# Optimization experiments

Hardware: AMD Instinct MI355X
Metric: run time of the kernel (lower is better)

The kernel has to match this reference:

```python
import jax, jax.numpy as jnp
import numpy as np

N, D, H, C, E = 16384, 768, 768, 2, 20

def setup_inputs() -> dict:
    key = jax.random.key(0)
    k1, k2, k3, k4, k5, k6 = jax.random.split(key, 6)
    return {
        "embeddings": jax.random.normal(k1, (N, D), dtype=jnp.float32),
        "component_idx": jax.random.randint(k2, (N,), 0, E, dtype=jnp.int64),
        "W1": jax.random.normal(k3, (E, D, H), dtype=jnp.float32) * (1.0 / np.sqrt(D)),
        "b1": jnp.zeros((E, H), dtype=jnp.float32),
        "W2": jax.random.normal(k4, (E, H, C), dtype=jnp.float32) * (1.0 / np.sqrt(H)),
        "b2": jnp.zeros((E, C), dtype=jnp.float32),
    }

def reference(embeddings, component_idx, W1, b1, W2, b2):
    # Each token n goes through expert component_idx[n]:
    #   y = relu(x @ W1[e] + b1[e]) @ W2[e] + b2[e]
    # The torch module's mask/cat/argsort reassembly is mathematically a
    # per-token select of its own expert's output at the original position.
    # Dense-expert formulation (standard jax MoE fallback), then gather.
    h = jax.nn.relu(jnp.einsum('nd,edh->enh', embeddings, W1) + b1[:, None, :])  # [E,N,H]
    y = jnp.einsum('enh,ehc->enc', h, W2) + b2[:, None, :]                        # [E,N,C]
    n_idx = jnp.arange(embeddings.shape[0])
    return y[component_idx, n_idx]  # [N,C]
```

## Files before the change

### kernel.cpp

```cpp
#include <hip/hip_runtime.h>

#define N_D 768
#define N_H 768
#define N_C 2
#define N_E 20
#define MT 128
#define NT 128
#define BK 32
#define KT (N_D / BK)
#define MAX_TILES 160
#define NCOL (N_H / NT)
#define ROWB (N_D * 2)
#define W1BLKS (N_E * (N_D / 64) * (N_H / 64))
#define XBBLKS 256

typedef __attribute__((ext_vector_type(8))) short short8;
typedef __attribute__((ext_vector_type(4))) float f32x4;

__device__ __forceinline__ unsigned short f2bf(float f) {
  unsigned u = __builtin_bit_cast(unsigned, f);
  u += 0x7FFFu + ((u >> 16) & 1u);
  return (unsigned short)(u >> 16);
}

#define GLD_LDS16(gp, lp)                                                        \
  __builtin_amdgcn_global_load_lds(                                              \
      (const __attribute__((address_space(1))) void*)(gp),                       \
      (__attribute__((address_space(3))) void*)(lp), 16, 0, 0)


__global__ __launch_bounds__(256) void k_prep(
    const int* __restrict__ cidx, int* __restrict__ counts,
    int* __restrict__ offsets, int* __restrict__ tiles,
    int* __restrict__ numTiles, int* __restrict__ sorted,
    const float* __restrict__ emb, unsigned short* __restrict__ Xb,
    const float* __restrict__ W1, unsigned short* __restrict__ W1t,
    float* __restrict__ out, int n) {
  const int tid = threadIdx.x;

  if (blockIdx.x == 0) {
    __shared__ int lc[4][N_E];
    __shared__ int tot[N_E];
    __shared__ int scur[N_E];
    const int w = tid >> 6;
    for (int k = tid; k < 4 * N_E; k += 256) ((int*)lc)[k] = 0;
    __syncthreads();
    const int4* c4 = (const int4*)cidx;
    const int nv = n >> 2;
    for (int i = tid; i < nv; i += 256) {
      int4 v = c4[i];
      int e0 = v.x < 0 ? 0 : (v.x >= N_E ? N_E - 1 : v.x);
      int e1 = v.y < 0 ? 0 : (v.y >= N_E ? N_E - 1 : v.y);
      int e2 = v.z < 0 ? 0 : (v.z >= N_E ? N_E - 1 : v.z);
      int e3 = v.w < 0 ? 0 : (v.w >= N_E ? N_E - 1 : v.w);
      atomicAdd(&lc[w][e0], 1);
      atomicAdd(&lc[w][e1], 1);
      atomicAdd(&lc[w][e2], 1);
      atomicAdd(&lc[w][e3], 1);
    }
    for (int i = (nv << 2) + tid; i < n; i += 256) {
      int e = cidx[i];
      e = e < 0 ? 0 : (e >= N_E ? N_E - 1 : e);
      atomicAdd(&lc[w][e], 1);
    }
    __syncthreads();
    if (tid < N_E) tot[tid] = lc[0][tid] + lc[1][tid] + lc[2][tid] + lc[3][tid];
    __syncthreads();
    if (tid < 64) {
      int lane = tid;
      int c = (lane < N_E) ? tot[lane] : 0;
      int nt = (c + MT - 1) / MT;
      int cs = c, ts = nt;
#pragma unroll
      for (int s = 1; s < 32; s <<= 1) {
        int t1 = __shfl_up(cs, s, 64);
        int t2 = __shfl_up(ts, s, 64);
        if (lane >= s) {
          cs += t1;
          ts += t2;
        }
      }
      int coff = cs - c;
      int tbase = ts - nt;
      if (lane < N_E) {
        counts[lane] = c;
        offsets[lane] = coff;
        scur[lane] = coff;
        for (int m = 0; m < nt; ++m) {
          int t = tbase + m;
          if (t < MAX_TILES) tiles[t] = (lane << 8) | m;
        }
      }
      if (lane == N_E - 1) *numTiles = ts > MAX_TILES ? MAX_TILES : ts;
    }
    __syncthreads();
    for (int i = tid; i < n; i += 256) {
      int e = cidx[i];
      e = e < 0 ? 0 : (e >= N_E ? N_E - 1 : e);
      int p = atomicAdd(&scur[e], 1);
      sorted[p] = i;
    }
    return;
  }

  if ((int)blockIdx.x < 1 + W1BLKS) {
    __shared__ float tile[64][65];
    int w1i = blockIdx.x - 1;
    int xcd = w1i & 7, ii = w1i >> 3;
    int wgid = xcd * (W1BLKS / 8) + ii;
    int e = wgid / 144;
    int rem = wgid - e * 144;
    int h0 = (rem % 12) * 64, d0 = (rem / 12) * 64;
    const float* src = W1 + (size_t)e * N_D * N_H;
    unsigned short* dst = W1t + (size_t)e * N_H * N_D;
    int tx = tid & 15, ty = tid >> 4;
#pragma unroll
    for (int s = 0; s < 4; ++s) {
      int d = s * 16 + ty;
      float4 v = *(const float4*)&src[(size_t)(d0 + d) * N_H + h0 + tx * 4];
      tile[d][tx * 4 + 0] = v.x;
      tile[d][tx * 4 + 1] = v.y;
      tile[d][tx * 4 + 2] = v.z;
      tile[d][tx * 4 + 3] = v.w;
    }
    __syncthreads();
    int px = tid & 7, py = tid >> 3;
#pragma unroll
    for (int s = 0; s < 2; ++s) {
      int h = s * 32 + py;
      short8 v;
#pragma unroll
      for (int j = 0; j < 8; ++j)
        v[j] = (short)f2bf(tile[px * 8 + j][h]);
      *(short8*)&dst[(size_t)(h0 + h) * N_D + d0 + px * 8] = v;
    }
    return;
  }

  int xb = blockIdx.x - 1 - W1BLKS;
  const float4* s4 = (const float4*)emb;
  ushort4* d4 = (ushort4*)Xb;
  const int total = n * (N_D / 4);
  for (int k = xb * 256 + tid; k < total; k += XBBLKS * 256) {
    float4 v = s4[k];
    ushort4 o;
    o.x = f2bf(v.x);
    o.y = f2bf(v.y);
    o.z = f2bf(v.z);
    o.w = f2bf(v.w);
    d4[k] = o;
  }
  if (xb < 8) {
    float4 zf = {0.f, 0.f, 0.f, 0.f};
    float4* of = (float4*)out;
    for (int k = xb * 256 + tid; k < n * N_C / 4; k += 8 * 256) of[k] = zf;
  }
}


__global__ __launch_bounds__(256, 2) void k_gemm(
    const unsigned short* __restrict__ Xb, const unsigned short* __restrict__ W1t,
    const float* __restrict__ b1, const float* __restrict__ W2,
    const float* __restrict__ b2, const int* __restrict__ sorted,
    const int* __restrict__ counts, const int* __restrict__ offsets,
    const int* __restrict__ tiles, const int* __restrict__ numTiles,
    float* __restrict__ out, int n) {
  const int nactive = *numTiles * NCOL;
  const int lin = (int)blockIdx.y * NCOL + (int)blockIdx.x;
  if (lin >= nactive) return;
  const int q = nactive >> 3, r = nactive & 7;
  const int c = lin & 7, ii = lin >> 3;
  const int wgid = (c < r ? c * (q + 1) : r * (q + 1) + (c - r) * q) + ii;
  const int tileIdx = wgid / NCOL;
  const int n0 = (wgid - tileIdx * NCOL) * NT;

  const int tv = tiles[tileIdx];
  const int e = tv >> 8;
  const int m0 = (tv & 255) * MT;
  const int off = offsets[e];
  const int cnt_rel = counts[e] - m0;

  __shared__ unsigned short lA[2][MT * BK];
  __shared__ unsigned short lB[2][NT * BK];

  const int tid = threadIdx.x;
  const int wid = tid >> 6, lane = tid & 63;
  const int wm = (wid >> 1) * 64, wn = (wid & 1) * 64;
  const int quad = lane >> 4, lm = lane & 15;

  const int R0 = wid * 32 + lm;
  const int pos0 = off + m0 + R0;
  const int pos1 = pos0 + 16;
  const int t0 = sorted[pos0 < n ? pos0 : 0];
  const int t1 = sorted[pos1 < n ? pos1 : 0];
  const char* agp0 = (const char*)Xb + (size_t)t0 * ROWB + quad * 16;
  const char* agp1 = (const char*)Xb + (size_t)t1 * ROWB + quad * 16;
  const char* bgp = (const char*)W1t + (size_t)e * N_H * ROWB +
                    (size_t)(n0 + R0) * ROWB + quad * 16;
  unsigned short* lap[2] = {&lA[0][(wid * 32) * BK], &lA[1][(wid * 32) * BK]};
  unsigned short* lbp[2] = {&lB[0][(wid * 32) * BK], &lB[1][(wid * 32) * BK]};

#define ISSUE_BATCH(kk, b)                                                       \
  do {                                                                           \
    const char* b_ = bgp + (kk)*64;                                              \
    GLD_LDS16(agp0 + (kk)*64, lap[b]);                                           \
    GLD_LDS16(agp1 + (kk)*64, lap[b] + 16 * BK);                                 \
    GLD_LDS16(b_, lbp[b]);                                                       \
    GLD_LDS16(b_ + 16 * ROWB, lbp[b] + 16 * BK);                                 \
  } while (0)

  f32x4 acc[4][4] = {};

  ISSUE_BATCH(0, 0);
  ISSUE_BATCH(1, 1);

  const int fa = quad * 128 + lm * 8;

  for (int kt = 0; kt < KT; ++kt) {
    const int cur = kt & 1;
    asm volatile("s_waitcnt vmcnt(4)\n\ts_barrier" ::: "memory");
    short8 af[4], bfr[4];
    for (int i = 0; i < 4; ++i)
      af[i] = *(const short8*)&lA[cur][((wm >> 4) + i) * 512 + fa];
    for (int j = 0; j < 4; ++j)
      bfr[j] = *(const short8*)&lB[cur][((wn >> 4) + j) * 512 + fa];
    asm volatile("s_waitcnt lgkmcnt(0)\n\ts_barrier" ::: "memory");
    int kk = kt + 2;
    if (kk >= KT) kk -= KT;
    ISSUE_BATCH(kk, cur);
    for (int i = 0; i < 4; ++i)
      for (int j = 0; j < 4; ++j)
        acc[i][j] =
            __builtin_amdgcn_mfma_f32_16x16x32_bf16(af[i], bfr[j], acc[i][j], 0, 0, 0);
  }

  float y0[4][4], y1[4][4];
  for (int i = 0; i < 4; ++i)
    for (int r2 = 0; r2 < 4; ++r2) y0[i][r2] = y1[i][r2] = 0.f;

  for (int j = 0; j < 4; ++j) {
    int col = n0 + wn + j * 16 + lm;
    float bias = b1[e * N_H + col];
    float2 w2 = *(const float2*)&W2[((size_t)e * N_H + col) * N_C];
    for (int i = 0; i < 4; ++i) {
      f32x4 a = acc[i][j];
      for (int r2 = 0; r2 < 4; ++r2) {
        float h = a[r2] + bias;
        h = h > 0.f ? h : 0.f;
        y0[i][r2] += h * w2.x;
        y1[i][r2] += h * w2.y;
      }
    }
  }
  for (int s = 1; s < 16; s <<= 1) {
    for (int i = 0; i < 4; ++i)
      for (int r2 = 0; r2 < 4; ++r2) {
        y0[i][r2] += __shfl_xor(y0[i][r2], s, 64);
        y1[i][r2] += __shfl_xor(y1[i][r2], s, 64);
      }
  }
  if (lm == 0) {
    const bool add_bias = (n0 == 0) && (wn == 0);
    float bb0 = add_bias ? b2[e * N_C + 0] : 0.f;
    float bb1 = add_bias ? b2[e * N_C + 1] : 0.f;
    for (int i = 0; i < 4; ++i) {
      for (int r2 = 0; r2 < 4; ++r2) {
        int mrel = wm + i * 16 + quad * 4 + r2;
        if (mrel < cnt_rel) {
          int token = sorted[off + m0 + mrel];
          atomicAdd(&out[(size_t)token * N_C + 0], y0[i][r2] + bb0);
          atomicAdd(&out[(size_t)token * N_C + 1], y1[i][r2] + bb1);
        }
      }
    }
  }
}


extern "C" void kernel_launch(void* const* d_in, const int* in_sizes, int n_in,
                              void* d_out, int out_size, void* d_ws, size_t ws_size,
                              hipStream_t stream) {
  const float* emb = (const float*)d_in[0];
  const int* cidx = (const int*)d_in[1];
  const float* W1 = (const float*)d_in[2];
  const float* b1 = (const float*)d_in[3];
  const float* W2 = (const float*)d_in[4];
  const float* b2 = (const float*)d_in[5];
  float* out = (float*)d_out;
  const int n = in_sizes[1];

  char* ws = (char*)d_ws;
  int* counts = (int*)ws;
  int* offsets = (int*)(ws + 128);
  int* numTiles = (int*)(ws + 384);
  int* tiles = (int*)(ws + 512);
  int* sorted = (int*)(ws + 2048);
  size_t sorted_bytes = ((size_t)n * 4 + 255) & ~(size_t)255;
  unsigned short* Xb = (unsigned short*)(ws + 2048 + sorted_bytes);
  unsigned short* W1t = Xb + (size_t)n * N_D;

  k_prep<<<1 + W1BLKS + XBBLKS, 256, 0, stream>>>(
      cidx, counts, offsets, tiles, numTiles, sorted, emb, Xb, W1, W1t, out, n);
  k_gemm<<<dim3(NCOL, MAX_TILES), 256, 0, stream>>>(
      Xb, W1t, b1, W2, b2, sorted, counts, offsets, tiles, numTiles, out, n);
}
```

Measured before the change: 212.6 us.

## Pre-gather tokens into expert-sorted MFMA-tiled layout, split prep into two kernels

Moves the token gather out of the GEMM. A new middle kernel writes bf16 activations in expert-sorted, 16-row groups padded to tile boundaries, and writes W1 in a matching fragment-contiguous group layout. The GEMM then loads A and B tiles with contiguous, coalesced 1KB-strided loads instead of per-row gathered loads. The cost is an extra kernel launch and serialization: the histogram and sort now run in a single-block kernel before the gather can start, so that work no longer overlaps with the W1 conversion.

Result: faster. 207.1 us (-2.6%).

```diff
diff --git a/kernel.cpp b/kernel.cpp
--- a/kernel.cpp
+++ b/kernel.cpp
@@ -10,9 +10,9 @@
 #define KT (N_D / BK)
 #define MAX_TILES 160
 #define NCOL (N_H / NT)
-#define ROWB (N_D * 2)
+#define GRPB 24576
+#define GPE (N_H / 16)
 #define W1BLKS (N_E * (N_D / 64) * (N_H / 64))
-#define XBBLKS 256
 
 typedef __attribute__((ext_vector_type(8))) short short8;
 typedef __attribute__((ext_vector_type(4))) float f32x4;
@@ -29,90 +29,131 @@
       (__attribute__((address_space(3))) void*)(lp), 16, 0, 0)
 
 
-__global__ __launch_bounds__(256) void k_prep(
-    const int* __restrict__ cidx, int* __restrict__ counts,
-    int* __restrict__ offsets, int* __restrict__ tiles,
-    int* __restrict__ numTiles, int* __restrict__ sorted,
-    const float* __restrict__ emb, unsigned short* __restrict__ Xb,
-    const float* __restrict__ W1, unsigned short* __restrict__ W1t,
-    float* __restrict__ out, int n) {
+__global__ __launch_bounds__(256) void k_front(const int* __restrict__ cidx,
+                                               int* __restrict__ counts,
+                                               int* __restrict__ offsets,
+                                               int* __restrict__ tiles,
+                                               int* __restrict__ numTiles,
+                                               int* __restrict__ ptotal,
+                                               int* __restrict__ sorted, int n) {
+  __shared__ int lc[4][N_E];
+  __shared__ int tot[N_E];
+  __shared__ int scur[N_E];
   const int tid = threadIdx.x;
-
-  if (blockIdx.x == 0) {
-    __shared__ int lc[4][N_E];
-    __shared__ int tot[N_E];
-    __shared__ int scur[N_E];
-    const int w = tid >> 6;
-    for (int k = tid; k < 4 * N_E; k += 256) ((int*)lc)[k] = 0;
-    __syncthreads();
-    const int4* c4 = (const int4*)cidx;
-    const int nv = n >> 2;
-    for (int i = tid; i < nv; i += 256) {
-      int4 v = c4[i];
-      int e0 = v.x < 0 ? 0 : (v.x >= N_E ? N_E - 1 : v.x);
-      int e1 = v.y < 0 ? 0 : (v.y >= N_E ? N_E - 1 : v.y);
-      int e2 = v.z < 0 ? 0 : (v.z >= N_E ? N_E - 1 : v.z);
-      int e3 = v.w < 0 ? 0 : (v.w >= N_E ? N_E - 1 : v.w);
-      atomicAdd(&lc[w][e0], 1);
-      atomicAdd(&lc[w][e1], 1);
-      atomicAdd(&lc[w][e2], 1);
-      atomicAdd(&lc[w][e3], 1);
-    }
-    for (int i = (nv << 2) + tid; i < n; i += 256) {
-      int e = cidx[i];
-      e = e < 0 ? 0 : (e >= N_E ? N_E - 1 : e);
-      atomicAdd(&lc[w][e], 1);
-    }
-    __syncthreads();
-    if (tid < N_E) tot[tid] = lc[0][tid] + lc[1][tid] + lc[2][tid] + lc[3][tid];
-    __syncthreads();
-    if (tid < 64) {
-      int lane = tid;
-      int c = (lane < N_E) ? tot[lane] : 0;
-      int nt = (c + MT - 1) / MT;
-      int cs = c, ts = nt;
-#pragma unroll
-      for (int s = 1; s < 32; s <<= 1) {
-        int t1 = __shfl_up(cs, s, 64);
-        int t2 = __shfl_up(ts, s, 64);
-        if (lane >= s) {
-          cs += t1;
-          ts += t2;
-        }
-      }
-      int coff = cs - c;
-      int tbase = ts - nt;
-      if (lane < N_E) {
-        counts[lane] = c;
-        offsets[lane] = coff;
-        scur[lane] = coff;
-        for (int m = 0; m < nt; ++m) {
-          int t = tbase + m;
-          if (t < MAX_TILES) tiles[t] = (lane << 8) | m;
-        }
-      }
-      if (lane == N_E - 1) *numTiles = ts > MAX_TILES ? MAX_TILES : ts;
-    }
-    __syncthreads();
-    for (int i = tid; i < n; i += 256) {
-      int e = cidx[i];
-      e = e < 0 ? 0 : (e >= N_E ? N_E - 1 : e);
-      int p = atomicAdd(&scur[e], 1);
-      sorted[p] = i;
+  const int w = tid >> 6;
+  for (int k = tid; k < 4 * N_E; k += 256) ((int*)lc)[k] = 0;
+  __syncthreads();
+  const int4* c4 = (const int4*)cidx;
+  const int nv = n >> 2;
+  for (int i = tid; i < nv; i += 256) {
+    int4 v = c4[i];
+    int e0 = v.x < 0 ? 0 : (v.x >= N_E ? N_E - 1 : v.x);
+    int e1 = v.y < 0 ? 0 : (v.y >= N_E ? N_E - 1 : v.y);
+    int e2 = v.z < 0 ? 0 : (v.z >= N_E ? N_E - 1 : v.z);
+    int e3 = v.w < 0 ? 0 : (v.w >= N_E ? N_E - 1 : v.w);
+    atomicAdd(&lc[w][e0], 1);
+    atomicAdd(&lc[w][e1], 1);
+    atomicAdd(&lc[w][e2], 1);
+    atomicAdd(&lc[w][e3], 1);
+  }
+  for (int i = (nv << 2) + tid; i < n; i += 256) {
+    int e = cidx[i];
+    e = e < 0 ? 0 : (e >= N_E ? N_E - 1 : e);
+    atomicAdd(&lc[w][e], 1);
+  }
+  __syncthreads();
+  if (tid < N_E) tot[tid] = lc[0][tid] + lc[1][tid] + lc[2][tid] + lc[3][tid];
+  __syncthreads();
+  if (tid < 64) {
+    int lane = tid;
+    int c = (lane < N_E) ? tot[lane] : 0;
+    int nt = (c + MT - 1) / MT;
+    int pad = nt * MT;
+    int ps = pad, ts = nt;
+#pragma unroll
+    for (int s = 1; s < 32; s <<= 1) {
+      int t1 = __shfl_up(ps, s, 64);
+      int t2 = __shfl_up(ts, s, 64);
+      if (lane >= s) {
+        ps += t1;
+        ts += t2;
+      }
+    }
+    int off = ps - pad;
+    int tbase = ts - nt;
+    if (lane < N_E) {
+      counts[lane] = c;
+      offsets[lane] = off;
+      scur[lane] = off;
+      for (int m = 0; m < nt; ++m) {
+        int t = tbase + m;
+        if (t < MAX_TILES) tiles[t] = (lane << 8) | m;
+      }
+      for (int p = off + c; p < off + pad; ++p) sorted[p] = -1;
+    }
+    if (lane == N_E - 1) {
+      *numTiles = ts > MAX_TILES ? MAX_TILES : ts;
+      *ptotal = ps;
+    }
+  }
+  __syncthreads();
+  for (int i = tid; i < n; i += 256) {
+    int e = cidx[i];
+    e = e < 0 ? 0 : (e >= N_E ? N_E - 1 : e);
+    int p = atomicAdd(&scur[e], 1);
+    sorted[p] = i;
+  }
+}
+
+
+__global__ __launch_bounds__(256) void k_mid(
+    const int* __restrict__ sorted, const int* __restrict__ ptotal,
+    const float* __restrict__ emb, unsigned short* __restrict__ Xs,
+    const float* __restrict__ W1, unsigned short* __restrict__ W1s,
+    float* __restrict__ out, int n, int nbg) {
+  const int tid = threadIdx.x;
+
+  if ((int)blockIdx.x < nbg) {
+    const int g = blockIdx.x;
+    if (g * 16 >= *ptotal) return;
+    const int row = tid & 15;
+    const int p0 = tid >> 4;
+    const int t = sorted[g * 16 + row];
+    const bool valid = t >= 0;
+    const float* src = emb + (size_t)(valid ? t : 0) * N_D;
+    unsigned short* dst = (unsigned short*)((char*)Xs + (size_t)g * GRPB);
+#pragma unroll
+    for (int it = 0; it < 6; ++it) {
+      int piece = p0 + 16 * it;
+      int kt = piece >> 2, ch = piece & 3;
+      int k0 = kt * 32 + ch * 8;
+      short8 v = {};
+      if (valid) {
+        float4 a = *(const float4*)(src + k0);
+        float4 b = *(const float4*)(src + k0 + 4);
+        v[0] = (short)f2bf(a.x);
+        v[1] = (short)f2bf(a.y);
+        v[2] = (short)f2bf(a.z);
+        v[3] = (short)f2bf(a.w);
+        v[4] = (short)f2bf(b.x);
+        v[5] = (short)f2bf(b.y);
+        v[6] = (short)f2bf(b.z);
+        v[7] = (short)f2bf(b.w);
+      }
+      *(short8*)(dst + (size_t)kt * 512 + ch * 128 + row * 8) = v;
     }
     return;
   }
 
-  if ((int)blockIdx.x < 1 + W1BLKS) {
+  if ((int)blockIdx.x < nbg + W1BLKS) {
     __shared__ float tile[64][65];
-    int w1i = blockIdx.x - 1;
+    int w1i = blockIdx.x - nbg;
     int xcd = w1i & 7, ii = w1i >> 3;
     int wgid = xcd * (W1BLKS / 8) + ii;
     int e = wgid / 144;
     int rem = wgid - e * 144;
     int h0 = (rem % 12) * 64, d0 = (rem / 12) * 64;
     const float* src = W1 + (size_t)e * N_D * N_H;
-    unsigned short* dst = W1t + (size_t)e * N_H * N_D;
     int tx = tid & 15, ty = tid >> 4;
 #pragma unroll
     for (int s = 0; s < 4; ++s) {
@@ -124,47 +165,35 @@
       tile[d][tx * 4 + 3] = v.w;
     }
     __syncthreads();
-    int px = tid & 7, py = tid >> 3;
 #pragma unroll
     for (int s = 0; s < 2; ++s) {
-      int h = s * 32 + py;
+      int piece = tid + 256 * s;
+      int g2 = piece >> 7, ktl = (piece >> 6) & 1, ch = (piece >> 4) & 3,
+          row = piece & 15;
       short8 v;
 #pragma unroll
       for (int j = 0; j < 8; ++j)
-        v[j] = (short)f2bf(tile[px * 8 + j][h]);
-      *(short8*)&dst[(size_t)(h0 + h) * N_D + d0 + px * 8] = v;
+        v[j] = (short)f2bf(tile[ktl * 32 + ch * 8 + j][g2 * 16 + row]);
+      char* dst = (char*)W1s + ((size_t)e * GPE + (h0 >> 4) + g2) * GRPB +
+                  ((d0 >> 5) + ktl) * 1024 + ch * 256 + row * 16;
+      *(short8*)dst = v;
     }
     return;
   }
 
-  int xb = blockIdx.x - 1 - W1BLKS;
-  const float4* s4 = (const float4*)emb;
-  ushort4* d4 = (ushort4*)Xb;
-  const int total = n * (N_D / 4);
-  for (int k = xb * 256 + tid; k < total; k += XBBLKS * 256) {
-    float4 v = s4[k];
-    ushort4 o;
-    o.x = f2bf(v.x);
-    o.y = f2bf(v.y);
-    o.z = f2bf(v.z);
-    o.w = f2bf(v.w);
-    d4[k] = o;
-  }
-  if (xb < 8) {
-    float4 zf = {0.f, 0.f, 0.f, 0.f};
-    float4* of = (float4*)out;
-    for (int k = xb * 256 + tid; k < n * N_C / 4; k += 8 * 256) of[k] = zf;
-  }
+  float4 zf = {0.f, 0.f, 0.f, 0.f};
+  float4* of = (float4*)out;
+  for (int k = tid; k < N_C * n / 4; k += 256) of[k] = zf;
 }
 
 
 __global__ __launch_bounds__(256, 2) void k_gemm(
-    const unsigned short* __restrict__ Xb, const unsigned short* __restrict__ W1t,
+    const unsigned short* __restrict__ Xs, const unsigned short* __restrict__ W1s,
     const float* __restrict__ b1, const float* __restrict__ W2,
     const float* __restrict__ b2, const int* __restrict__ sorted,
     const int* __restrict__ counts, const int* __restrict__ offsets,
     const int* __restrict__ tiles, const int* __restrict__ numTiles,
-    float* __restrict__ out, int n) {
+    float* __restrict__ out) {
   const int nactive = *numTiles * NCOL;
   const int lin = (int)blockIdx.y * NCOL + (int)blockIdx.x;
   if (lin >= nactive) return;
@@ -188,25 +217,19 @@
   const int wm = (wid >> 1) * 64, wn = (wid & 1) * 64;
   const int quad = lane >> 4, lm = lane & 15;
 
-  const int R0 = wid * 32 + lm;
-  const int pos0 = off + m0 + R0;
-  const int pos1 = pos0 + 16;
-  const int t0 = sorted[pos0 < n ? pos0 : 0];
-  const int t1 = sorted[pos1 < n ? pos1 : 0];
-  const char* agp0 = (const char*)Xb + (size_t)t0 * ROWB + quad * 16;
-  const char* agp1 = (const char*)Xb + (size_t)t1 * ROWB + quad * 16;
-  const char* bgp = (const char*)W1t + (size_t)e * N_H * ROWB +
-                    (size_t)(n0 + R0) * ROWB + quad * 16;
+  const char* agp =
+      (const char*)Xs + ((size_t)((off + m0) >> 4) + 2 * wid) * GRPB + lane * 16;
+  const char* bgp = (const char*)W1s +
+                    ((size_t)e * GPE + (n0 >> 4) + 2 * wid) * GRPB + lane * 16;
   unsigned short* lap[2] = {&lA[0][(wid * 32) * BK], &lA[1][(wid * 32) * BK]};
   unsigned short* lbp[2] = {&lB[0][(wid * 32) * BK], &lB[1][(wid * 32) * BK]};
 
 #define ISSUE_BATCH(kk, b)                                                       \
   do {                                                                           \
-    const char* b_ = bgp + (kk)*64;                                              \
-    GLD_LDS16(agp0 + (kk)*64, lap[b]);                                           \
-    GLD_LDS16(agp1 + (kk)*64, lap[b] + 16 * BK);                                 \
-    GLD_LDS16(b_, lbp[b]);                                                       \
-    GLD_LDS16(b_ + 16 * ROWB, lbp[b] + 16 * BK);                                 \
+    GLD_LDS16(agp + (kk)*1024, lap[b]);                                          \
+    GLD_LDS16(agp + GRPB + (kk)*1024, lap[b] + 512);                             \
+    GLD_LDS16(bgp + (kk)*1024, lbp[b]);                                          \
+    GLD_LDS16(bgp + GRPB + (kk)*1024, lbp[b] + 512);                             \
   } while (0)
 
   f32x4 acc[4][4] = {};
@@ -293,14 +316,19 @@
   int* counts = (int*)ws;
   int* offsets = (int*)(ws + 128);
   int* numTiles = (int*)(ws + 384);
+  int* ptotal = (int*)(ws + 388);
   int* tiles = (int*)(ws + 512);
   int* sorted = (int*)(ws + 2048);
-  size_t sorted_bytes = ((size_t)n * 4 + 255) & ~(size_t)255;
-  unsigned short* Xb = (unsigned short*)(ws + 2048 + sorted_bytes);
-  unsigned short* W1t = Xb + (size_t)n * N_D;
-
-  k_prep<<<1 + W1BLKS + XBBLKS, 256, 0, stream>>>(
-      cidx, counts, offsets, tiles, numTiles, sorted, emb, Xb, W1, W1t, out, n);
+  const int pcap = n + N_E * MT;
+  const int nbg = (pcap + 15) / 16;
+  size_t sorted_bytes = ((size_t)nbg * 16 * 4 + 255) & ~(size_t)255;
+  unsigned short* Xs = (unsigned short*)(ws + 2048 + sorted_bytes);
+  unsigned short* W1s = Xs + (size_t)nbg * 16 * N_D;
+
+  k_front<<<1, 256, 0, stream>>>(cidx, counts, offsets, tiles, numTiles, ptotal,
+                                 sorted, n);
+  k_mid<<<nbg + W1BLKS + 1, 256, 0, stream>>>(sorted, ptotal, emb, Xs, W1, W1s,
+                                              out, n, nbg);
   k_gemm<<<dim3(NCOL, MAX_TILES), 256, 0, stream>>>(
-      Xb, W1t, b1, W2, b2, sorted, counts, offsets, tiles, numTiles, out, n);
-}
+      Xs, W1s, b1, W2, b2, sorted, counts, offsets, tiles, numTiles, out);
+}
```
